# Performance work log

Measured on AMD Instinct MI355X. Metric: run time of the kernel, lower is better.

The kernel has to match this reference:

```python
import jax, jax.numpy as jnp
import numpy as np

E = 8          # num_experts
K = 2          # top-k experts per token
CAP_RATIO = 1.05


def setup_inputs() -> dict:
    key = jax.random.key(0)
    k0, k1, k2, k3 = jax.random.split(key, 4)
    B, S, D, H = 2, 2048, 512, 2048
    return {
        "x": jax.random.normal(k0, (B, S, D), jnp.float32),
        "gate_w": jax.random.normal(k1, (E, D), jnp.float32) * (1.0 / np.sqrt(D)),
        "fc1_w": jax.random.normal(k2, (E, D, H), jnp.float32) * (1.0 / np.sqrt(D)),
        "fc1_b": jnp.zeros((E, H), jnp.float32),
        "fc2_w": jax.random.normal(k3, (E, H, D), jnp.float32) * (1.0 / np.sqrt(H)),
        "fc2_b": jnp.zeros((E, D), jnp.float32),
    }


def reference(x, gate_w, fc1_w, fc1_b, fc2_w, fc2_b):
    B, S, D = x.shape
    xf = x.reshape(-1, D)               # [T, D]
    T = xf.shape[0]

    # ---- router (eval mode: no noise) ----
    logits = xf @ gate_w.T              # [T, E]
    gates = jax.nn.softmax(logits, axis=-1)
    top_g, top_i = jax.lax.top_k(gates, K)   # [T, K]

    # importance auxiliary loss (std unbiased=False == jnp.std default)
    imp = gates.sum(axis=0)                  # [E]
    imp_loss = (jnp.std(imp) / (imp.mean() + 1e-6)) ** 2

    # ---- capacity-limited dispatch mask ----
    # torch loops slot-major: slot 0 over all tokens in order, then slot 1.
    # position of each (slot, token) entry within its expert's queue:
    buffer_cap = round(K * T * CAP_RATIO / E)
    idx_sm = top_i.T.reshape(-1)                        # [K*T] slot-major
    oh = jax.nn.one_hot(idx_sm, E, dtype=jnp.int32)     # [K*T, E]
    pos = jnp.cumsum(oh, axis=0) - oh                   # earlier same-expert count
    pos_e = jnp.take_along_axis(pos, idx_sm[:, None], axis=1)[:, 0]
    within = (pos_e < buffer_cap).reshape(K, T).T       # [T, K] bool

    wf = within.astype(xf.dtype)
    oh_tke = jax.nn.one_hot(top_i, E, dtype=xf.dtype) * wf[..., None]  # dispatch mask [T,K,E]
    combine_te = jnp.einsum('tk,tke->te', top_g * wf, oh_tke / jnp.maximum(oh_tke, 1e-30) * oh_tke) if False else jnp.einsum('tk,tke->te', top_g * wf, jax.nn.one_hot(top_i, E, dtype=xf.dtype))

    # load-balance loss from post-capacity token counts
    tokens_per_expert = oh_tke.sum(axis=(0, 1))         # [E]
    l_load = (jnp.std(tokens_per_expert) / (tokens_per_expert.mean() + 1e-6)) ** 2
    l_aux = 0.5 * (imp_loss + l_load)

    # ---- per-expert MLP (dense compute, masked combine) ----
    h = jnp.einsum('td,edh->teh', xf, fc1_w) + fc1_b[None]      # [T, E, H]
    h = jax.nn.gelu(h, approximate=False)                       # torch nn.GELU default
    y = jnp.einsum('teh,ehd->ted', h, fc2_w) + fc2_b[None]      # [T, E, D]

    out = jnp.einsum('te,ted->td', combine_te, y).reshape(B, S, D)
    return out, l_aux, l_load
```

## Files before the change

### kernel.cpp

```cpp
#include <hip/hip_runtime.h>
#include <hip/hip_bf16.h>

#define E_    8
#define TT    4096
#define DD    512
#define HH    2048
#define CAP   1075
#define MPAD  1152
#define MT    9
#define MT2   18

typedef __bf16 bf16_t;
typedef bf16_t bf16x4 __attribute__((ext_vector_type(4)));
typedef bf16_t bf16x8 __attribute__((ext_vector_type(8)));
typedef float  f32x4  __attribute__((ext_vector_type(4)));
typedef unsigned int u32;

__device__ __forceinline__ bf16_t tobf(float f) { return (bf16_t)f; }

__device__ __forceinline__ float gelu_f(float v) {
  const float u = v * (0.7978845608028654f + 0.035677408136300125f * v * v);
  const float a = __builtin_fabsf(u);
  const float ex = __expf(2.0f * a);
  float th = 1.0f - 2.0f / (ex + 1.0f);
  th = __builtin_copysignf(th, u);
  return 0.5f * v * (1.0f + th);
}

#define OFF_TOPI  256u
#define OFF_TOPG  (OFF_TOPI + 4096u*2u*4u)
#define OFF_SLOT  (OFF_TOPG + 4096u*2u*4u)
#define OFF_ETOK  (OFF_SLOT + 4096u*2u*4u)
#define OFF_EWT   (OFF_ETOK + 8u*1152u*4u)
#define OFF_XG    (OFF_EWT  + 8u*1152u*4u)
#define XG_BYTES  (8u*1152u*512u*2u)
#define OFF_W1T   (OFF_XG + XG_BYTES)
#define W1T_BYTES (8u*512u*2048u*2u)
#define OFF_W2T   (OFF_W1T + W1T_BYTES)
#define W2T_BYTES (8u*2048u*512u*2u)
#define OFF_H     (OFF_W2T + W2T_BYTES)
#define H_BYTES   (8u*1152u*2048u*2u)
#define OFF_Y     OFF_XG

__global__ __launch_bounds__(256) void router_kernel(
    const float* __restrict__ x, const float* __restrict__ gw,
    float* __restrict__ imp, int* __restrict__ top_i, float* __restrict__ top_g) {
  const int tid = threadIdx.x;
  const int wid = tid >> 6, lane = tid & 63;
  const int t = blockIdx.x * 4 + wid;

  float p[E_];
#pragma unroll
  for (int e = 0; e < E_; ++e) p[e] = 0.f;
  const float* xr = x + (size_t)t * DD;
#pragma unroll
  for (int it = 0; it < DD / 64; ++it) {
    const int d = it * 64 + lane;
    const float xv = xr[d];
#pragma unroll
    for (int e = 0; e < E_; ++e) p[e] += xv * gw[e * DD + d];
  }
#pragma unroll
  for (int off = 32; off > 0; off >>= 1) {
#pragma unroll
    for (int e = 0; e < E_; ++e) p[e] += __shfl_down(p[e], off);
  }

  __shared__ float simp[4][E_];
  if (lane == 0) {
    float mx = p[0];
#pragma unroll
    for (int e = 1; e < E_; ++e) mx = fmaxf(mx, p[e]);
    float g[E_]; float s = 0.f;
#pragma unroll
    for (int e = 0; e < E_; ++e) { g[e] = expf(p[e] - mx); s += g[e]; }
    const float inv = 1.f / s;
#pragma unroll
    for (int e = 0; e < E_; ++e) { g[e] *= inv; simp[wid][e] = g[e]; }
    int i0 = 0;
#pragma unroll
    for (int e = 1; e < E_; ++e) if (g[e] > g[i0]) i0 = e;
    int i1 = (i0 == 0) ? 1 : 0;
#pragma unroll
    for (int e = 0; e < E_; ++e) if (e != i0 && g[e] > g[i1]) i1 = e;
    top_i[t * 2 + 0] = i0;  top_i[t * 2 + 1] = i1;
    top_g[t * 2 + 0] = g[i0]; top_g[t * 2 + 1] = g[i1];
  }
  __syncthreads();
  if (tid < E_) {
    const float s = simp[0][tid] + simp[1][tid] + simp[2][tid] + simp[3][tid];
    atomicAdd(&imp[tid], s);
  }
}

__global__ __launch_bounds__(1024) void capacity_kernel(
    const int* __restrict__ top_i, const float* __restrict__ top_g,
    const float* __restrict__ imp, int* __restrict__ etok, float* __restrict__ ewt,
    int* __restrict__ slot_map, int* __restrict__ kept, float* __restrict__ scal) {
  __shared__ u32 wt[16][4];
  const int tid = threadIdx.x, wave = tid >> 6, lane = tid & 63;

  int eidx[8];
#pragma unroll
  for (int q = 0; q < 8; ++q) {
    const int j = tid * 8 + q;
    const int k = j >> 12, t = j & (TT - 1);
    eidx[q] = top_i[t * 2 + k];
  }
  u32 pk[4] = {0u, 0u, 0u, 0u};
#pragma unroll
  for (int q = 0; q < 8; ++q) pk[eidx[q] >> 1] += 1u << ((eidx[q] & 1) * 16);

  u32 v[4] = {pk[0], pk[1], pk[2], pk[3]};
#pragma unroll
  for (int off = 1; off < 64; off <<= 1) {
#pragma unroll
    for (int p = 0; p < 4; ++p) {
      const u32 n = (u32)__shfl_up((int)v[p], off);
      if (lane >= off) v[p] += n;
    }
  }
  if (lane == 63) {
#pragma unroll
    for (int p = 0; p < 4; ++p) wt[wave][p] = v[p];
  }
  __syncthreads();
  u32 base[4] = {0u, 0u, 0u, 0u}, tot[4] = {0u, 0u, 0u, 0u};
#pragma unroll
  for (int w = 0; w < 16; ++w) {
#pragma unroll
    for (int p = 0; p < 4; ++p) {
      const u32 x = wt[w][p];
      if (w < wave) base[p] += x;
      tot[p] += x;
    }
  }
  int run[E_];
#pragma unroll
  for (int p = 0; p < 4; ++p) {
    const u32 excl = base[p] + v[p] - pk[p];
    run[2 * p]     = (int)(excl & 0xFFFFu);
    run[2 * p + 1] = (int)(excl >> 16);
  }
#pragma unroll
  for (int q = 0; q < 8; ++q) {
    const int e = eidx[q];
    const int pos = run[e]++;
    const int j = tid * 8 + q;
    if (pos < CAP) {
      const int k = j >> 12, t = j & (TT - 1);
      etok[e * MPAD + pos] = t;
      ewt[e * MPAD + pos] = top_g[t * 2 + k];
      slot_map[j] = (e << 16) | pos;
    } else {
      slot_map[j] = -1;
    }
  }
  if (tid == 0) {
    float tpe[E_];
#pragma unroll
    for (int p = 0; p < 4; ++p) {
      const int t0 = (int)(tot[p] & 0xFFFFu), t1 = (int)(tot[p] >> 16);
      const int k0 = t0 < CAP ? t0 : CAP, k1 = t1 < CAP ? t1 : CAP;
      kept[2 * p] = k0; kept[2 * p + 1] = k1;
      tpe[2 * p] = (float)k0; tpe[2 * p + 1] = (float)k1;
    }
    float ms = 0.f;
#pragma unroll
    for (int e = 0; e < E_; ++e) ms += tpe[e];
    ms *= (1.f / E_);
    float vt = 0.f;
#pragma unroll
    for (int e = 0; e < E_; ++e) { const float d = tpe[e] - ms; vt += d * d; }
    vt *= (1.f / E_);
    const float ll = vt / ((ms + 1e-6f) * (ms + 1e-6f));

    float iv[E_], mi = 0.f;
#pragma unroll
    for (int e = 0; e < E_; ++e) { iv[e] = imp[e]; mi += iv[e]; }
    mi *= (1.f / E_);
    float vi = 0.f;
#pragma unroll
    for (int e = 0; e < E_; ++e) { const float d = iv[e] - mi; vi += d * d; }
    vi *= (1.f / E_);
    const float il = vi / ((mi + 1e-6f) * (mi + 1e-6f));

    scal[0] = 0.5f * (il + ll);
    scal[1] = ll;
  }
}

__global__ __launch_bounds__(256) void gather_kernel(
    const float* __restrict__ x, const int* __restrict__ etok,
    const int* __restrict__ kept, bf16_t* __restrict__ Xg) {
  const int e = blockIdx.y, wid = threadIdx.x >> 6, lane = threadIdx.x & 63;
  const int m = blockIdx.x * 4 + wid;
  if (m >= kept[e]) return;
  const int t = etok[e * MPAD + m];
  const float* src = x + (size_t)t * DD + lane * 8;
  const float4 a = *(const float4*)src;
  const float4 b = *(const float4*)(src + 4);
  bf16_t tmp[8] = {tobf(a.x), tobf(a.y), tobf(a.z), tobf(a.w),
                   tobf(b.x), tobf(b.y), tobf(b.z), tobf(b.w)};
  *(bf16x8*)(Xg + ((size_t)e * MPAD + m) * DD + lane * 8) = *(const bf16x8*)tmp;
}

__global__ __launch_bounds__(256) void transpose_both_kernel(
    const float* __restrict__ fc1, bf16_t* __restrict__ w1t,
    const float* __restrict__ fc2, bf16_t* __restrict__ w2t) {
  __shared__ float tile[32][33];
  const int z = blockIdx.z;
  const bool first = (z < 8);
  const int e = first ? z : z - 8;
  const int R = first ? DD : HH;
  const int C = first ? HH : DD;
  const int ct = first ? blockIdx.x : blockIdx.y;
  const int rt = first ? blockIdx.y : blockIdx.x;
  const float* ip = (first ? fc1 : fc2) + (size_t)e * DD * HH;
  bf16_t* op = (first ? w1t : w2t) + (size_t)e * DD * HH;
  const int r0 = rt * 32, c0 = ct * 32;
  const int tx = threadIdx.x, ty = threadIdx.y;
#pragma unroll
  for (int i = 0; i < 4; ++i)
    tile[ty + i * 8][tx] = ip[(size_t)(r0 + ty + i * 8) * C + c0 + tx];
  __syncthreads();
#pragma unroll
  for (int i = 0; i < 4; ++i)
    op[(size_t)(c0 + ty + i * 8) * R + r0 + tx] = tobf(tile[tx][ty + i * 8]);
}

template <int MI, int KLEN, int KSTR>
__device__ __forceinline__ void gemm_core(
    const bf16_t* __restrict__ A, const bf16_t* __restrict__ B,
    bf16_t* As, bf16_t* Bs, f32x4 (&acc)[4][MI]) {
  const int tid = threadIdx.x;
  const int wave = tid >> 6, lane = tid & 63;
  const int r8 = lane >> 3;
  const int kswz = ((lane & 7) ^ r8) * 8;
  const bf16_t* ga = A + (size_t)(wave * (MI * 8) + r8) * KSTR + kswz;
  const bf16_t* gb = B + (size_t)(wave * 32 + r8) * KSTR + kswz;
  const int mw = (wave >> 1) * (MI * 16), nw = (wave & 1) * 64;
  const int l15 = lane & 15, quad = lane >> 4;
  const int sw = l15 & 7;

  for (int k0 = 0; k0 < KLEN; k0 += 64) {
    __syncthreads();
#pragma unroll
    for (int p = 0; p < MI; ++p) {
      __builtin_amdgcn_global_load_lds(
          (const __attribute__((address_space(1))) void*)(ga + (size_t)p * 8 * KSTR + k0),
          (__attribute__((address_space(3))) void*)(As + (wave * (MI * 8) + p * 8) * 64),
          16, 0, 0);
    }
#pragma unroll
    for (int p = 0; p < 4; ++p) {
      __builtin_amdgcn_global_load_lds(
          (const __attribute__((address_space(1))) void*)(gb + (size_t)p * 8 * KSTR + k0),
          (__attribute__((address_space(3))) void*)(Bs + (wave * 32 + p * 8) * 64),
          16, 0, 0);
    }
    __syncthreads();
#pragma unroll
    for (int ks = 0; ks < 2; ++ks) {
      bf16x8 af[MI], bfr[4];
#pragma unroll
      for (int i = 0; i < MI; ++i)
        af[i] = *(const bf16x8*)(As + (mw + i * 16 + l15) * 64 + (((ks * 4 + quad) ^ sw) << 3));
#pragma unroll
      for (int j = 0; j < 4; ++j)
        bfr[j] = *(const bf16x8*)(Bs + (nw + j * 16 + l15) * 64 + (((ks * 4 + quad) ^ sw) << 3));
#pragma unroll
      for (int j = 0; j < 4; ++j)
#pragma unroll
        for (int i = 0; i < MI; ++i)
          acc[j][i] = __builtin_amdgcn_mfma_f32_16x16x32_bf16(bfr[j], af[i], acc[j][i], 0, 0, 0);
    }
  }
}

__global__ __launch_bounds__(256, 3) void gemm1_kernel(
    const bf16_t* __restrict__ Xg, const bf16_t* __restrict__ W1t,
    const float* __restrict__ b1, bf16_t* __restrict__ Hbuf) {
  __shared__ __align__(16) bf16_t As[128 * 64];
  __shared__ __align__(16) bf16_t Bs[128 * 64];
  const int e = blockIdx.x, tileN = blockIdx.y, tileM = blockIdx.z;
  const bf16_t* A = Xg + ((size_t)e * MPAD + tileM * 128) * DD;
  const bf16_t* B = W1t + ((size_t)e * HH + tileN * 128) * DD;
  f32x4 acc[4][4];
  const f32x4 z = {0.f, 0.f, 0.f, 0.f};
#pragma unroll
  for (int j = 0; j < 4; ++j)
#pragma unroll
    for (int i = 0; i < 4; ++i) acc[j][i] = z;
  gemm_core<4, DD, DD>(A, B, As, Bs, acc);

  const int tid = threadIdx.x, wave = tid >> 6, lane = tid & 63;
  const int mw = (wave >> 1) * 64, nw = (wave & 1) * 64;
  const int l15 = lane & 15, quad = lane >> 4;
#pragma unroll
  for (int j = 0; j < 4; ++j) {
    const int n0 = tileN * 128 + nw + j * 16 + quad * 4;
    const float4 b4 = *(const float4*)(b1 + e * HH + n0);
#pragma unroll
    for (int i = 0; i < 4; ++i) {
      const int m = tileM * 128 + mw + i * 16 + l15;
      bf16x4 h4;
      h4.x = tobf(gelu_f(acc[j][i][0] + b4.x));
      h4.y = tobf(gelu_f(acc[j][i][1] + b4.y));
      h4.z = tobf(gelu_f(acc[j][i][2] + b4.z));
      h4.w = tobf(gelu_f(acc[j][i][3] + b4.w));
      *(bf16x4*)(Hbuf + ((size_t)e * MPAD + m) * HH + n0) = h4;
    }
  }
}

__global__ __launch_bounds__(256, 5) void gemm2_kernel(
    const bf16_t* __restrict__ Hbuf, const bf16_t* __restrict__ W2t,
    const int* __restrict__ kept, float* __restrict__ Ybuf) {
  __shared__ __align__(16) bf16_t As[64 * 64];
  __shared__ __align__(16) bf16_t Bs[128 * 64];
  const int e = blockIdx.x, tileN = blockIdx.y, tileM = blockIdx.z;
  const bf16_t* A = Hbuf + ((size_t)e * MPAD + tileM * 64) * HH;
  const bf16_t* B = W2t + ((size_t)e * DD + tileN * 128) * HH;
  f32x4 acc[4][2];
  const f32x4 z = {0.f, 0.f, 0.f, 0.f};
#pragma unroll
  for (int j = 0; j < 4; ++j)
#pragma unroll
    for (int i = 0; i < 2; ++i) acc[j][i] = z;
  gemm_core<2, HH, HH>(A, B, As, Bs, acc);

  const int tid = threadIdx.x, wave = tid >> 6, lane = tid & 63;
  const int mw = (wave >> 1) * 32, nw = (wave & 1) * 64;
  const int l15 = lane & 15, quad = lane >> 4;
  const int nk = kept[e];
#pragma unroll
  for (int j = 0; j < 4; ++j) {
    const int n0 = tileN * 128 + nw + j * 16 + quad * 4;
#pragma unroll
    for (int i = 0; i < 2; ++i) {
      const int m = tileM * 64 + mw + i * 16 + l15;
      if (m < nk)
        *(f32x4*)(Ybuf + ((size_t)e * MPAD + m) * DD + n0) = acc[j][i];
    }
  }
}

__global__ __launch_bounds__(128) void combine_kernel(
    const float* __restrict__ Ybuf, const float* __restrict__ b2,
    const int* __restrict__ slot_map, const float* __restrict__ top_g,
    float* __restrict__ out) {
  const int t = blockIdx.x;
  const int c = threadIdx.x * 4;
  float4 acc = {0.f, 0.f, 0.f, 0.f};
#pragma unroll
  for (int k = 0; k < 2; ++k) {
    const int sm = slot_map[k * TT + t];
    if (sm >= 0) {
      const int e = sm >> 16, pos = sm & 0xFFFF;
      const float w = top_g[t * 2 + k];
      const float4 y = *(const float4*)(Ybuf + ((size_t)e * MPAD + pos) * DD + c);
      const float4 bb = *(const float4*)(b2 + e * DD + c);
      acc.x += w * (y.x + bb.x);
      acc.y += w * (y.y + bb.y);
      acc.z += w * (y.z + bb.z);
      acc.w += w * (y.w + bb.w);
    }
  }
  *(float4*)(out + (size_t)t * DD + c) = acc;
}

extern "C" void kernel_launch(void* const* d_in, const int* in_sizes, int n_in,
                              void* d_out, int out_size, void* d_ws, size_t ws_size,
                              hipStream_t stream) {
  const float* x      = (const float*)d_in[0];
  const float* gate_w = (const float*)d_in[1];
  const float* fc1_w  = (const float*)d_in[2];
  const float* fc1_b  = (const float*)d_in[3];
  const float* fc2_w  = (const float*)d_in[4];
  const float* fc2_b  = (const float*)d_in[5];
  float* out = (float*)d_out;

  char* ws = (char*)d_ws;
  float*  imp   = (float*)(ws + 0);
  int*    kept  = (int*)(ws + 64);
  int*    top_i = (int*)(ws + OFF_TOPI);
  float*  top_g = (float*)(ws + OFF_TOPG);
  int*    slotm = (int*)(ws + OFF_SLOT);
  int*    etok  = (int*)(ws + OFF_ETOK);
  float*  ewt   = (float*)(ws + OFF_EWT);
  bf16_t* Xg    = (bf16_t*)(ws + OFF_XG);
  bf16_t* W1t   = (bf16_t*)(ws + OFF_W1T);
  bf16_t* W2t   = (bf16_t*)(ws + OFF_W2T);
  bf16_t* Hbuf  = (bf16_t*)(ws + OFF_H);
  float*  Ybuf  = (float*)(ws + OFF_Y);

  hipMemsetAsync(ws, 0, 256, stream);

  transpose_both_kernel<<<dim3(64, 16, 16), dim3(32, 8), 0, stream>>>(fc1_w, W1t, fc2_w, W2t);

  router_kernel<<<TT / 4, 256, 0, stream>>>(x, gate_w, imp, top_i, top_g);
  capacity_kernel<<<1, 1024, 0, stream>>>(top_i, top_g, imp, etok, ewt, slotm, kept,
                                          out + (size_t)TT * DD);
  gather_kernel<<<dim3(MPAD / 4, E_), 256, 0, stream>>>(x, etok, kept, Xg);

  gemm1_kernel<<<dim3(E_, HH / 128, MT), 256, 0, stream>>>(Xg, W1t, fc1_b, Hbuf);
  gemm2_kernel<<<dim3(E_, DD / 128, MT2), 256, 0, stream>>>(Hbuf, W2t, kept, Ybuf);
  combine_kernel<<<TT, 128, 0, stream>>>(Ybuf, fc2_b, slotm, top_g, out);
}
```

Before: 231.1 us.

## Fuse router, capacity and gather into one cooperative kernel; widen transpose; bf16 Y

Router, capacity scan and token gather are merged into a single cooperative kernel of 64 blocks that uses grid-wide syncs instead of three separate launches. The weight transpose switches to 64x64 tiles with vectorised bf16x4 stores. The second GEMM now writes its output in bf16 and the combine kernel reads bf16, halving Y traffic at some cost in precision. Cooperative launch limits parallelism to 64 blocks, and only one of them does the capacity scan.

```diff
diff --git a/kernel.cpp b/kernel.cpp
--- a/kernel.cpp
+++ b/kernel.cpp
@@ -1,5 +1,8 @@
 #include <hip/hip_runtime.h>
 #include <hip/hip_bf16.h>
+#include <hip/hip_cooperative_groups.h>
+
+namespace cg = cooperative_groups;
 
 #define E_    8
 #define TT    4096
@@ -42,173 +45,182 @@
 #define H_BYTES   (8u*1152u*2048u*2u)
 #define OFF_Y     OFF_XG
 
-__global__ __launch_bounds__(256) void router_kernel(
+__global__ __launch_bounds__(1024) void prep_kernel(
     const float* __restrict__ x, const float* __restrict__ gw,
-    float* __restrict__ imp, int* __restrict__ top_i, float* __restrict__ top_g) {
-  const int tid = threadIdx.x;
-  const int wid = tid >> 6, lane = tid & 63;
-  const int t = blockIdx.x * 4 + wid;
-
-  float p[E_];
-#pragma unroll
-  for (int e = 0; e < E_; ++e) p[e] = 0.f;
-  const float* xr = x + (size_t)t * DD;
-#pragma unroll
-  for (int it = 0; it < DD / 64; ++it) {
-    const int d = it * 64 + lane;
-    const float xv = xr[d];
-#pragma unroll
-    for (int e = 0; e < E_; ++e) p[e] += xv * gw[e * DD + d];
-  }
-#pragma unroll
-  for (int off = 32; off > 0; off >>= 1) {
-#pragma unroll
-    for (int e = 0; e < E_; ++e) p[e] += __shfl_down(p[e], off);
-  }
-
-  __shared__ float simp[4][E_];
+    float* __restrict__ imp, int* __restrict__ top_i, float* __restrict__ top_g,
+    int* __restrict__ etok, float* __restrict__ ewt, int* __restrict__ slot_map,
+    int* __restrict__ kept, float* __restrict__ scal, bf16_t* __restrict__ Xg) {
+  const int tid = threadIdx.x, bid = blockIdx.x;
+  const int wave = tid >> 6, lane = tid & 63;
+  __shared__ float simp[16][E_];
+  __shared__ u32 wt[16][4];
+
+  float limp[E_];
+#pragma unroll
+  for (int e = 0; e < E_; ++e) limp[e] = 0.f;
+  for (int pass = 0; pass < 4; ++pass) {
+    const int t = pass * 1024 + bid * 16 + wave;
+    float p[E_];
+#pragma unroll
+    for (int e = 0; e < E_; ++e) p[e] = 0.f;
+    const float* xr = x + (size_t)t * DD;
+#pragma unroll
+    for (int it = 0; it < DD / 64; ++it) {
+      const int d = it * 64 + lane;
+      const float xv = xr[d];
+#pragma unroll
+      for (int e = 0; e < E_; ++e) p[e] += xv * gw[e * DD + d];
+    }
+#pragma unroll
+    for (int off = 32; off > 0; off >>= 1) {
+#pragma unroll
+      for (int e = 0; e < E_; ++e) p[e] += __shfl_down(p[e], off);
+    }
+    if (lane == 0) {
+      float mx = p[0];
+#pragma unroll
+      for (int e = 1; e < E_; ++e) mx = fmaxf(mx, p[e]);
+      float g[E_]; float s = 0.f;
+#pragma unroll
+      for (int e = 0; e < E_; ++e) { g[e] = expf(p[e] - mx); s += g[e]; }
+      const float inv = 1.f / s;
+#pragma unroll
+      for (int e = 0; e < E_; ++e) { g[e] *= inv; limp[e] += g[e]; }
+      int i0 = 0;
+#pragma unroll
+      for (int e = 1; e < E_; ++e) if (g[e] > g[i0]) i0 = e;
+      int i1 = (i0 == 0) ? 1 : 0;
+#pragma unroll
+      for (int e = 0; e < E_; ++e) if (e != i0 && g[e] > g[i1]) i1 = e;
+      top_i[t * 2 + 0] = i0;  top_i[t * 2 + 1] = i1;
+      top_g[t * 2 + 0] = g[i0]; top_g[t * 2 + 1] = g[i1];
+    }
+  }
   if (lane == 0) {
-    float mx = p[0];
-#pragma unroll
-    for (int e = 1; e < E_; ++e) mx = fmaxf(mx, p[e]);
-    float g[E_]; float s = 0.f;
-#pragma unroll
-    for (int e = 0; e < E_; ++e) { g[e] = expf(p[e] - mx); s += g[e]; }
-    const float inv = 1.f / s;
-#pragma unroll
-    for (int e = 0; e < E_; ++e) { g[e] *= inv; simp[wid][e] = g[e]; }
-    int i0 = 0;
-#pragma unroll
-    for (int e = 1; e < E_; ++e) if (g[e] > g[i0]) i0 = e;
-    int i1 = (i0 == 0) ? 1 : 0;
-#pragma unroll
-    for (int e = 0; e < E_; ++e) if (e != i0 && g[e] > g[i1]) i1 = e;
-    top_i[t * 2 + 0] = i0;  top_i[t * 2 + 1] = i1;
-    top_g[t * 2 + 0] = g[i0]; top_g[t * 2 + 1] = g[i1];
+#pragma unroll
+    for (int e = 0; e < E_; ++e) simp[wave][e] = limp[e];
   }
   __syncthreads();
   if (tid < E_) {
-    const float s = simp[0][tid] + simp[1][tid] + simp[2][tid] + simp[3][tid];
+    float s = 0.f;
+#pragma unroll
+    for (int w = 0; w < 16; ++w) s += simp[w][tid];
     atomicAdd(&imp[tid], s);
   }
-}
-
-__global__ __launch_bounds__(1024) void capacity_kernel(
-    const int* __restrict__ top_i, const float* __restrict__ top_g,
-    const float* __restrict__ imp, int* __restrict__ etok, float* __restrict__ ewt,
-    int* __restrict__ slot_map, int* __restrict__ kept, float* __restrict__ scal) {
-  __shared__ u32 wt[16][4];
-  const int tid = threadIdx.x, wave = tid >> 6, lane = tid & 63;
-
-  int eidx[8];
-#pragma unroll
-  for (int q = 0; q < 8; ++q) {
-    const int j = tid * 8 + q;
-    const int k = j >> 12, t = j & (TT - 1);
-    eidx[q] = top_i[t * 2 + k];
-  }
-  u32 pk[4] = {0u, 0u, 0u, 0u};
-#pragma unroll
-  for (int q = 0; q < 8; ++q) pk[eidx[q] >> 1] += 1u << ((eidx[q] & 1) * 16);
-
-  u32 v[4] = {pk[0], pk[1], pk[2], pk[3]};
-#pragma unroll
-  for (int off = 1; off < 64; off <<= 1) {
+  cg::this_grid().sync();
+
+  if (bid == 0) {
+    int eidx[8];
+#pragma unroll
+    for (int q = 0; q < 8; ++q) {
+      const int j = tid * 8 + q;
+      const int k = j >> 12, t = j & (TT - 1);
+      eidx[q] = top_i[t * 2 + k];
+    }
+    u32 pk[4] = {0u, 0u, 0u, 0u};
+#pragma unroll
+    for (int q = 0; q < 8; ++q) pk[eidx[q] >> 1] += 1u << ((eidx[q] & 1) * 16);
+
+    u32 v[4] = {pk[0], pk[1], pk[2], pk[3]};
+#pragma unroll
+    for (int off = 1; off < 64; off <<= 1) {
+#pragma unroll
+      for (int p = 0; p < 4; ++p) {
+        const u32 n = (u32)__shfl_up((int)v[p], off);
+        if (lane >= off) v[p] += n;
+      }
+    }
+    if (lane == 63) {
+#pragma unroll
+      for (int p = 0; p < 4; ++p) wt[wave][p] = v[p];
+    }
+    __syncthreads();
+    u32 base[4] = {0u, 0u, 0u, 0u}, tot[4] = {0u, 0u, 0u, 0u};
+#pragma unroll
+    for (int w = 0; w < 16; ++w) {
+#pragma unroll
+      for (int p = 0; p < 4; ++p) {
+        const u32 xv = wt[w][p];
+        if (w < wave) base[p] += xv;
+        tot[p] += xv;
+      }
+    }
+    int run[E_];
 #pragma unroll
     for (int p = 0; p < 4; ++p) {
-      const u32 n = (u32)__shfl_up((int)v[p], off);
-      if (lane >= off) v[p] += n;
-    }
-  }
-  if (lane == 63) {
-#pragma unroll
-    for (int p = 0; p < 4; ++p) wt[wave][p] = v[p];
-  }
-  __syncthreads();
-  u32 base[4] = {0u, 0u, 0u, 0u}, tot[4] = {0u, 0u, 0u, 0u};
-#pragma unroll
-  for (int w = 0; w < 16; ++w) {
-#pragma unroll
-    for (int p = 0; p < 4; ++p) {
-      const u32 x = wt[w][p];
-      if (w < wave) base[p] += x;
-      tot[p] += x;
-    }
-  }
-  int run[E_];
-#pragma unroll
-  for (int p = 0; p < 4; ++p) {
-    const u32 excl = base[p] + v[p] - pk[p];
-    run[2 * p]     = (int)(excl & 0xFFFFu);
-    run[2 * p + 1] = (int)(excl >> 16);
-  }
-#pragma unroll
-  for (int q = 0; q < 8; ++q) {
-    const int e = eidx[q];
-    const int pos = run[e]++;
-    const int j = tid * 8 + q;
-    if (pos < CAP) {
-      const int k = j >> 12, t = j & (TT - 1);
-      etok[e * MPAD + pos] = t;
-      ewt[e * MPAD + pos] = top_g[t * 2 + k];
-      slot_map[j] = (e << 16) | pos;
-    } else {
-      slot_map[j] = -1;
-    }
-  }
-  if (tid == 0) {
-    float tpe[E_];
-#pragma unroll
-    for (int p = 0; p < 4; ++p) {
-      const int t0 = (int)(tot[p] & 0xFFFFu), t1 = (int)(tot[p] >> 16);
-      const int k0 = t0 < CAP ? t0 : CAP, k1 = t1 < CAP ? t1 : CAP;
-      kept[2 * p] = k0; kept[2 * p + 1] = k1;
-      tpe[2 * p] = (float)k0; tpe[2 * p + 1] = (float)k1;
-    }
-    float ms = 0.f;
-#pragma unroll
-    for (int e = 0; e < E_; ++e) ms += tpe[e];
-    ms *= (1.f / E_);
-    float vt = 0.f;
-#pragma unroll
-    for (int e = 0; e < E_; ++e) { const float d = tpe[e] - ms; vt += d * d; }
-    vt *= (1.f / E_);
-    const float ll = vt / ((ms + 1e-6f) * (ms + 1e-6f));
-
-    float iv[E_], mi = 0.f;
-#pragma unroll
-    for (int e = 0; e < E_; ++e) { iv[e] = imp[e]; mi += iv[e]; }
-    mi *= (1.f / E_);
-    float vi = 0.f;
-#pragma unroll
-    for (int e = 0; e < E_; ++e) { const float d = iv[e] - mi; vi += d * d; }
-    vi *= (1.f / E_);
-    const float il = vi / ((mi + 1e-6f) * (mi + 1e-6f));
-
-    scal[0] = 0.5f * (il + ll);
-    scal[1] = ll;
-  }
-}
-
-__global__ __launch_bounds__(256) void gather_kernel(
-    const float* __restrict__ x, const int* __restrict__ etok,
-    const int* __restrict__ kept, bf16_t* __restrict__ Xg) {
-  const int e = blockIdx.y, wid = threadIdx.x >> 6, lane = threadIdx.x & 63;
-  const int m = blockIdx.x * 4 + wid;
-  if (m >= kept[e]) return;
-  const int t = etok[e * MPAD + m];
-  const float* src = x + (size_t)t * DD + lane * 8;
-  const float4 a = *(const float4*)src;
-  const float4 b = *(const float4*)(src + 4);
-  bf16_t tmp[8] = {tobf(a.x), tobf(a.y), tobf(a.z), tobf(a.w),
-                   tobf(b.x), tobf(b.y), tobf(b.z), tobf(b.w)};
-  *(bf16x8*)(Xg + ((size_t)e * MPAD + m) * DD + lane * 8) = *(const bf16x8*)tmp;
+      const u32 excl = base[p] + v[p] - pk[p];
+      run[2 * p]     = (int)(excl & 0xFFFFu);
+      run[2 * p + 1] = (int)(excl >> 16);
+    }
+#pragma unroll
+    for (int q = 0; q < 8; ++q) {
+      const int e = eidx[q];
+      const int pos = run[e]++;
+      const int j = tid * 8 + q;
+      if (pos < CAP) {
+        const int k = j >> 12, t = j & (TT - 1);
+        etok[e * MPAD + pos] = t;
+        ewt[e * MPAD + pos] = top_g[t * 2 + k];
+        slot_map[j] = (e << 16) | pos;
+      } else {
+        slot_map[j] = -1;
+      }
+    }
+    if (tid == 0) {
+      float tpe[E_];
+#pragma unroll
+      for (int p = 0; p < 4; ++p) {
+        const int t0 = (int)(tot[p] & 0xFFFFu), t1 = (int)(tot[p] >> 16);
+        const int k0 = t0 < CAP ? t0 : CAP, k1 = t1 < CAP ? t1 : CAP;
+        kept[2 * p] = k0; kept[2 * p + 1] = k1;
+        tpe[2 * p] = (float)k0; tpe[2 * p + 1] = (float)k1;
+      }
+      float ms = 0.f;
+#pragma unroll
+      for (int e = 0; e < E_; ++e) ms += tpe[e];
+      ms *= (1.f / E_);
+      float vt = 0.f;
+#pragma unroll
+      for (int e = 0; e < E_; ++e) { const float d = tpe[e] - ms; vt += d * d; }
+      vt *= (1.f / E_);
+      const float ll = vt / ((ms + 1e-6f) * (ms + 1e-6f));
+
+      float iv[E_], mi = 0.f;
+#pragma unroll
+      for (int e = 0; e < E_; ++e) { iv[e] = imp[e]; mi += iv[e]; }
+      mi *= (1.f / E_);
+      float vi = 0.f;
+#pragma unroll
+      for (int e = 0; e < E_; ++e) { const float d = iv[e] - mi; vi += d * d; }
+      vi *= (1.f / E_);
+      const float il = vi / ((mi + 1e-6f) * (mi + 1e-6f));
+
+      scal[0] = 0.5f * (il + ll);
+      scal[1] = ll;
+    }
+  }
+  cg::this_grid().sync();
+
+#pragma unroll
+  for (int i = 0; i < 9; ++i) {
+    const int rw = i * 1024 + bid * 16 + wave;
+    const int e = rw / MPAD, m = rw % MPAD;
+    if (m < kept[e]) {
+      const int t = etok[e * MPAD + m];
+      const float* src = x + (size_t)t * DD + lane * 8;
+      const float4 a = *(const float4*)src;
+      const float4 b = *(const float4*)(src + 4);
+      bf16_t tmp[8] = {tobf(a.x), tobf(a.y), tobf(a.z), tobf(a.w),
+                       tobf(b.x), tobf(b.y), tobf(b.z), tobf(b.w)};
+      *(bf16x8*)(Xg + ((size_t)e * MPAD + m) * DD + lane * 8) = *(const bf16x8*)tmp;
+    }
+  }
 }
 
 __global__ __launch_bounds__(256) void transpose_both_kernel(
     const float* __restrict__ fc1, bf16_t* __restrict__ w1t,
     const float* __restrict__ fc2, bf16_t* __restrict__ w2t) {
-  __shared__ float tile[32][33];
+  __shared__ float tile[64][65];
   const int z = blockIdx.z;
   const bool first = (z < 8);
   const int e = first ? z : z - 8;
@@ -218,15 +230,24 @@
   const int rt = first ? blockIdx.y : blockIdx.x;
   const float* ip = (first ? fc1 : fc2) + (size_t)e * DD * HH;
   bf16_t* op = (first ? w1t : w2t) + (size_t)e * DD * HH;
-  const int r0 = rt * 32, c0 = ct * 32;
-  const int tx = threadIdx.x, ty = threadIdx.y;
-#pragma unroll
-  for (int i = 0; i < 4; ++i)
-    tile[ty + i * 8][tx] = ip[(size_t)(r0 + ty + i * 8) * C + c0 + tx];
+  const int r0 = rt * 64, c0 = ct * 64;
+  const int tid = threadIdx.x;
+  const int rr = tid >> 6, cc = tid & 63;
+#pragma unroll
+  for (int p = 0; p < 16; ++p)
+    tile[p * 4 + rr][cc] = ip[(size_t)(r0 + p * 4 + rr) * C + c0 + cc];
   __syncthreads();
-#pragma unroll
-  for (int i = 0; i < 4; ++i)
-    op[(size_t)(c0 + ty + i * 8) * R + r0 + tx] = tobf(tile[tx][ty + i * 8]);
+  const int g = tid & 15, ob = tid >> 4;
+#pragma unroll
+  for (int p = 0; p < 4; ++p) {
+    const int oc = p * 16 + ob;
+    bf16x4 o4;
+    o4.x = tobf(tile[g * 4 + 0][oc]);
+    o4.y = tobf(tile[g * 4 + 1][oc]);
+    o4.z = tobf(tile[g * 4 + 2][oc]);
+    o4.w = tobf(tile[g * 4 + 3][oc]);
+    *(bf16x4*)(op + (size_t)(c0 + oc) * R + r0 + g * 4) = o4;
+  }
 }
 
 template <int MI, int KLEN, int KSTR>
@@ -316,7 +337,7 @@
 
 __global__ __launch_bounds__(256, 5) void gemm2_kernel(
     const bf16_t* __restrict__ Hbuf, const bf16_t* __restrict__ W2t,
-    const int* __restrict__ kept, float* __restrict__ Ybuf) {
+    const int* __restrict__ kept, bf16_t* __restrict__ Ybuf) {
   __shared__ __align__(16) bf16_t As[64 * 64];
   __shared__ __align__(16) bf16_t Bs[128 * 64];
   const int e = blockIdx.x, tileN = blockIdx.y, tileM = blockIdx.z;
@@ -340,14 +361,20 @@
 #pragma unroll
     for (int i = 0; i < 2; ++i) {
       const int m = tileM * 64 + mw + i * 16 + l15;
-      if (m < nk)
-        *(f32x4*)(Ybuf + ((size_t)e * MPAD + m) * DD + n0) = acc[j][i];
+      if (m < nk) {
+        bf16x4 o4;
+        o4.x = tobf(acc[j][i][0]);
+        o4.y = tobf(acc[j][i][1]);
+        o4.z = tobf(acc[j][i][2]);
+        o4.w = tobf(acc[j][i][3]);
+        *(bf16x4*)(Ybuf + ((size_t)e * MPAD + m) * DD + n0) = o4;
+      }
     }
   }
 }
 
 __global__ __launch_bounds__(128) void combine_kernel(
-    const float* __restrict__ Ybuf, const float* __restrict__ b2,
+    const bf16_t* __restrict__ Ybuf, const float* __restrict__ b2,
     const int* __restrict__ slot_map, const float* __restrict__ top_g,
     float* __restrict__ out) {
   const int t = blockIdx.x;
@@ -359,12 +386,12 @@
     if (sm >= 0) {
       const int e = sm >> 16, pos = sm & 0xFFFF;
       const float w = top_g[t * 2 + k];
-      const float4 y = *(const float4*)(Ybuf + ((size_t)e * MPAD + pos) * DD + c);
+      const bf16x4 y4 = *(const bf16x4*)(Ybuf + ((size_t)e * MPAD + pos) * DD + c);
       const float4 bb = *(const float4*)(b2 + e * DD + c);
-      acc.x += w * (y.x + bb.x);
-      acc.y += w * (y.y + bb.y);
-      acc.z += w * (y.z + bb.z);
-      acc.w += w * (y.w + bb.w);
+      acc.x += w * ((float)y4.x + bb.x);
+      acc.y += w * ((float)y4.y + bb.y);
+      acc.z += w * ((float)y4.z + bb.z);
+      acc.w += w * ((float)y4.w + bb.w);
     }
   }
   *(float4*)(out + (size_t)t * DD + c) = acc;
@@ -393,16 +420,17 @@
   bf16_t* W1t   = (bf16_t*)(ws + OFF_W1T);
   bf16_t* W2t   = (bf16_t*)(ws + OFF_W2T);
   bf16_t* Hbuf  = (bf16_t*)(ws + OFF_H);
-  float*  Ybuf  = (float*)(ws + OFF_Y);
+  bf16_t* Ybuf  = (bf16_t*)(ws + OFF_Y);
+  float*  scal  = out + (size_t)TT * DD;
 
   hipMemsetAsync(ws, 0, 256, stream);
 
-  transpose_both_kernel<<<dim3(64, 16, 16), dim3(32, 8), 0, stream>>>(fc1_w, W1t, fc2_w, W2t);
-
-  router_kernel<<<TT / 4, 256, 0, stream>>>(x, gate_w, imp, top_i, top_g);
-  capacity_kernel<<<1, 1024, 0, stream>>>(top_i, top_g, imp, etok, ewt, slotm, kept,
-                                          out + (size_t)TT * DD);
-  gather_kernel<<<dim3(MPAD / 4, E_), 256, 0, stream>>>(x, etok, kept, Xg);
+  transpose_both_kernel<<<dim3(32, 8, 16), 256, 0, stream>>>(fc1_w, W1t, fc2_w, W2t);
+
+  void* args[] = {(void*)&x, (void*)&gate_w, (void*)&imp, (void*)&top_i,
+                  (void*)&top_g, (void*)&etok, (void*)&ewt, (void*)&slotm,
+                  (void*)&kept, (void*)&scal, (void*)&Xg};
+  hipLaunchCooperativeKernel((void*)prep_kernel, dim3(64), dim3(1024), args, 0, stream);
 
   gemm1_kernel<<<dim3(E_, HH / 128, MT), 256, 0, stream>>>(Xg, W1t, fc1_b, Hbuf);
   gemm2_kernel<<<dim3(E_, DD / 128, MT2), 256, 0, stream>>>(Hbuf, W2t, kept, Ybuf);
```

New measurement: 271.1 us. +17.3%, slower.
